# Performance work log

Hardware: AMD Instinct MI355X
Metric: run time of the kernel (lower is better)

Reference implementation:

```python
import jax, jax.numpy as jnp
import numpy as np

B, A, F, T = 4096, 64, 124, 8
H1, H2 = 64, 16


def setup_inputs() -> dict:
    key = jax.random.key(0)
    ks = jax.random.split(key, 10)
    x = jax.random.normal(ks[0], (B, A, F + 1), dtype=jnp.float32)
    types = jax.random.randint(ks[1], (B, A), 0, T).astype(jnp.float32)
    x = x.at[:, :, 0].set(types)  # column 0 stores atom-type index
    mask = (jax.random.uniform(ks[2], (B, A)) < 0.9).astype(jnp.float32)
    s1 = 1.0 / np.sqrt(F)
    s2 = 1.0 / np.sqrt(H1)
    s3 = 1.0 / np.sqrt(H2)
    return {
        "x_padded": x,
        "mask": mask,
        "W1": jax.random.normal(ks[3], (T, F, H1), dtype=jnp.float32) * s1,
        "b1": jax.random.normal(ks[4], (T, H1), dtype=jnp.float32) * s1,
        "W2": jax.random.normal(ks[5], (T, H1, H2), dtype=jnp.float32) * s2,
        "b2": jax.random.normal(ks[6], (T, H2), dtype=jnp.float32) * s2,
        "W3": jax.random.normal(ks[7], (T, H2, 1), dtype=jnp.float32) * s3,
        "b3": jax.random.normal(ks[8], (T, 1), dtype=jnp.float32) * s3,
    }


def reference(x_padded, mask, W1, b1, W2, b2, W3, b3):
    # x_padded: [B, A, 1+F]; mask: [B, A]
    type_idx = x_padded[:, :, 0].astype(jnp.int32)           # [B, A]
    feats = x_padded[:, :, 1:]                               # [B, A, F]
    n_types = W1.shape[0]
    # Faithful to the original: every type's subnet runs on the FULL batch
    # with non-matching atoms zero-masked (bias paths still contribute).
    type_mask = (type_idx[None, :, :] == jnp.arange(n_types)[:, None, None]).astype(feats.dtype)  # [T,B,A]
    sel = feats[None, :, :, :] * type_mask[..., None]        # [T,B,A,F]
    h = jax.nn.relu(jnp.einsum('tbaf,tfh->tbah', sel, W1) + b1[:, None, None, :])
    h = jax.nn.relu(jnp.einsum('tbah,thg->tbag', h, W2) + b2[:, None, None, :])
    o = jnp.einsum('tbag,tgo->tbao', h, W3) + b3[:, None, None, :]  # [T,B,A,1]
    per_atom = (o[..., 0] * mask[None, :, :]).sum(axis=0)   # [B, A]
    return per_atom.sum(axis=1, keepdims=True)               # [B, 1]
```

## Files before the change

### kernel.cpp

```cpp
#include <hip/hip_runtime.h>
#include <stdint.h>

#define NMOL 4096
#define NATOMS (NMOL * 64)
#define NF 124
#define NT 8
#define ROWV 125
#define CAP 65536

#define WS_DCONST  0
#define WS_CURSOR  64
#define WS_W1S     128
#define WS_W2T     131200
#define WS_LIST    147712

#define HS 72

typedef __attribute__((ext_vector_type(8))) short short8;
typedef __attribute__((ext_vector_type(4))) float floatx4;
typedef __attribute__((ext_vector_type(4), aligned(4))) float floatx4u;
typedef __attribute__((ext_vector_type(4))) unsigned int uint4v;

__device__ __forceinline__ unsigned short f2bf(float f) {
    unsigned u = __builtin_bit_cast(unsigned, f);
    u += 0x7fffu + ((u >> 16) & 1u);
    return (unsigned short)(u >> 16);
}
__device__ __forceinline__ unsigned pk2(float a, float b) {
    return (unsigned)f2bf(a) | ((unsigned)f2bf(b) << 16);
}
__device__ __forceinline__ void ld_lds16(const void* g, void* lds) {
    __builtin_amdgcn_global_load_lds(
        (const __attribute__((address_space(1))) unsigned int*)g,
        (__attribute__((address_space(3))) unsigned int*)lds, 16, 0, 0);
}

__global__ __launch_bounds__(256) void k_setup(const float* __restrict__ W1,
                                               const float* __restrict__ b1,
                                               const float* __restrict__ W2,
                                               const float* __restrict__ b2,
                                               const float* __restrict__ W3,
                                               const float* __restrict__ b3,
                                               float* __restrict__ dconst,
                                               unsigned* __restrict__ cursor,
                                               unsigned short* __restrict__ W1S,
                                               unsigned short* __restrict__ W2T,
                                               float* __restrict__ out) {
    int tid = threadIdx.x, b = blockIdx.x;
    if (b == 0) {
        __shared__ float c[NT];
        if (tid < 128) {
            int t = tid >> 4, g = tid & 15;
            float acc = b2[t * 16 + g];
            for (int h = 0; h < 64; ++h) {
                float h1 = b1[t * 64 + h];
                h1 = h1 > 0.f ? h1 : 0.f;
                acc += h1 * W2[(size_t)t * 1024 + h * 16 + g];
            }
            float h2 = acc > 0.f ? acc : 0.f;
            float v = h2 * W3[t * 16 + g];
            #pragma unroll
            for (int off = 1; off < 16; off <<= 1) v += __shfl_xor(v, off);
            if (g == 0) c[t] = v + b3[t];
        }
        if (tid < NT) cursor[tid] = (unsigned)(tid * CAP);
        __syncthreads();
        if (tid == 0) {
            float T_ = 0.f;
            for (int i = 0; i < NT; ++i) T_ += c[i];
            for (int i = 0; i < NT; ++i) dconst[i] = T_ - c[i] + b3[i];
        }
    } else if (b <= 8) {
        int t = b - 1;
        const float* w1g = W1 + (size_t)t * NF * 64;
        unsigned short* dst = W1S + (size_t)t * 8192;
        for (int id = tid; id < 1024; id += 256) {
            int h = id >> 4, cc = id & 15;
            unsigned u[4];
            #pragma unroll
            for (int j = 0; j < 4; ++j) {
                int f0 = cc * 8 + 2 * j;
                unsigned short lo = (f0 < NF)     ? f2bf(w1g[f0 * 64 + h])       : (unsigned short)0;
                unsigned short hi = (f0 + 1 < NF) ? f2bf(w1g[(f0 + 1) * 64 + h]) : (unsigned short)0;
                u[j] = (unsigned)lo | ((unsigned)hi << 16);
            }
            int p = cc ^ (h & 15);
            *(uint4v*)(dst + h * 128 + p * 8) = (uint4v){u[0], u[1], u[2], u[3]};
        }
        unsigned short* d2 = W2T + (size_t)t * 1024;
        for (int i = tid; i < 1024; i += 256) {
            int g = i >> 6, h = i & 63;
            d2[i] = f2bf(W2[(size_t)t * 1024 + h * 16 + g]);
        }
    } else {
        out[(b - 9) * 256 + tid] = 0.0f;
    }
}

__global__ __launch_bounds__(256) void k_sort(const float* __restrict__ x,
                                              const float* __restrict__ mask,
                                              unsigned* __restrict__ cursor,
                                              unsigned* __restrict__ list) {
    __shared__ unsigned scnt[2][4][NT];
    __shared__ unsigned sbase[2][4][NT];
    int tid = threadIdx.x;
    int wv = tid >> 6, lane = tid & 63;
    int base = blockIdx.x * 512;

    int ty_[2];
    unsigned long long mym[2];
    #pragma unroll
    for (int i = 0; i < 2; ++i) {
        int atom = base + i * 256 + tid;
        float tf = x[(size_t)atom * ROWV];
        float m  = mask[atom];
        int tt = (m != 0.0f) ? (int)tf : -1;
        ty_[i] = tt;
        unsigned long long bm = 0ull;
        unsigned mycnt = 0;
        #pragma unroll
        for (int ty = 0; ty < NT; ++ty) {
            unsigned long long b = __ballot(tt == ty);
            if (ty == tt) bm = b;
            if (lane == ty) mycnt = (unsigned)__popcll(b);
        }
        mym[i] = bm;
        if (lane < NT) scnt[i][wv][lane] = mycnt;
    }
    __syncthreads();
    if (tid < NT) {
        unsigned tot = 0;
        #pragma unroll
        for (int i = 0; i < 2; ++i)
            #pragma unroll
            for (int w = 0; w < 4; ++w) tot += scnt[i][w][tid];
        unsigned run = atomicAdd(&cursor[tid], tot);
        #pragma unroll
        for (int i = 0; i < 2; ++i)
            #pragma unroll
            for (int w = 0; w < 4; ++w) { sbase[i][w][tid] = run; run += scnt[i][w][tid]; }
    }
    __syncthreads();
    #pragma unroll
    for (int i = 0; i < 2; ++i) {
        int tt = ty_[i];
        if (tt >= 0) {
            unsigned rank = (unsigned)__popcll(mym[i] & ((1ull << lane) - 1ull));
            list[sbase[i][wv][tt] + rank] = (unsigned)(base + i * 256 + tid);
        }
    }
}

__global__ __launch_bounds__(256, 4) void k_mlp(const float* __restrict__ x,
                                                const unsigned short* __restrict__ W1S,
                                                const float* __restrict__ b1,
                                                const unsigned short* __restrict__ W2T,
                                                const float* __restrict__ b2,
                                                const float* __restrict__ W3,
                                                const unsigned* __restrict__ cursor,
                                                const float* __restrict__ dconst,
                                                const unsigned* __restrict__ list,
                                                float* __restrict__ out) {
    __shared__ unsigned short sW[64 * 128];
    __shared__ unsigned short sH[128 * HS];

    int t    = blockIdx.x >> 9;
    int tile = blockIdx.x & 511;
    int cnt  = (int)(cursor[t] - (unsigned)(t * CAP));
    int valid = cnt - (tile << 7);
    if (valid <= 0) return;
    if (valid > 128) valid = 128;
    int rowstart = t * CAP + (tile << 7);

    int tid  = threadIdx.x;
    int wv   = tid >> 6;
    int lane = tid & 63;
    int quad = lane >> 4, l15 = lane & 15;
    int rowbase = wv * 32;

    {
        const char* src = (const char*)W1S + (size_t)t * 16384 + wv * 4096 + lane * 16;
        char*       dst = (char*)sW + wv * 4096;
        #pragma unroll
        for (int i = 0; i < 4; ++i) ld_lds16(src + i * 1024, dst + i * 1024);
    }

    unsigned aid[2];
    #pragma unroll
    for (int m = 0; m < 2; ++m) {
        int row = rowbase + m * 16 + l15;
        aid[m] = list[rowstart + (row < valid ? row : 0)];
    }

    float b1v[4];
    #pragma unroll
    for (int n = 0; n < 4; ++n) b1v[n] = b1[t * 64 + n * 16 + l15];
    const unsigned short* w2t = W2T + (size_t)t * 1024;
    short8 bw2[2];
    #pragma unroll
    for (int ks = 0; ks < 2; ++ks)
        bw2[ks] = *(const short8*)(w2t + l15 * 64 + ks * 32 + quad * 8);
    float b2v = b2[t * 16 + l15];
    float w3v = W3[t * 16 + l15];
    float dct = dconst[t];

    short8 afrag[2][4];
    #pragma unroll
    for (int m = 0; m < 2; ++m) {
        const float* rp = x + (size_t)aid[m] * ROWV + 1;
        #pragma unroll
        for (int ks = 0; ks < 4; ++ks) {
            int k0 = ks * 32 + quad * 8;
            floatx4 f0 = (floatx4)(*(const floatx4u*)(rp + k0));
            floatx4 f1 = (floatx4)0.f;
            if (!(ks == 3 && quad == 3))
                f1 = (floatx4)(*(const floatx4u*)(rp + k0 + 4));
            uint4v uu = (uint4v){pk2(f0[0], f0[1]), pk2(f0[2], f0[3]),
                                 pk2(f1[0], f1[1]), pk2(f1[2], f1[3])};
            afrag[m][ks] = __builtin_bit_cast(short8, uu);
        }
    }

    __syncthreads();

    floatx4 c1[2][4];
    #pragma unroll
    for (int m = 0; m < 2; ++m)
        #pragma unroll
        for (int n = 0; n < 4; ++n) c1[m][n] = (floatx4)0.f;

    #pragma unroll
    for (int ks = 0; ks < 4; ++ks) {
        short8 bf[4];
        #pragma unroll
        for (int n = 0; n < 4; ++n)
            bf[n] = *(const short8*)(sW + (n * 16 + l15) * 128 + (((ks * 4 + quad) ^ l15) << 3));
        #pragma unroll
        for (int n = 0; n < 4; ++n) {
            c1[0][n] = __builtin_amdgcn_mfma_f32_16x16x32_bf16(afrag[0][ks], bf[n], c1[0][n], 0, 0, 0);
            c1[1][n] = __builtin_amdgcn_mfma_f32_16x16x32_bf16(afrag[1][ks], bf[n], c1[1][n], 0, 0, 0);
        }
    }

    #pragma unroll
    for (int m = 0; m < 2; ++m)
        #pragma unroll
        for (int n = 0; n < 4; ++n) {
            int col = n * 16 + l15;
            #pragma unroll
            for (int r = 0; r < 4; ++r) {
                float v = c1[m][n][r] + b1v[n];
                v = v > 0.f ? v : 0.f;
                sH[(rowbase + m * 16 + quad * 4 + r) * HS + col] = f2bf(v);
            }
        }

    floatx4 c2[2];
    c2[0] = (floatx4)0.f; c2[1] = (floatx4)0.f;
    #pragma unroll
    for (int ks = 0; ks < 2; ++ks) {
        int ko = ks * 32 + quad * 8;
        short8 a0 = *(const short8*)(sH + (rowbase + l15) * HS + ko);
        short8 a1 = *(const short8*)(sH + (rowbase + 16 + l15) * HS + ko);
        c2[0] = __builtin_amdgcn_mfma_f32_16x16x32_bf16(a0, bw2[ks], c2[0], 0, 0, 0);
        c2[1] = __builtin_amdgcn_mfma_f32_16x16x32_bf16(a1, bw2[ks], c2[1], 0, 0, 0);
    }

    #pragma unroll
    for (int m = 0; m < 2; ++m) {
        float h2v[4];
        #pragma unroll
        for (int r = 0; r < 4; ++r) {
            float v = c2[m][r] + b2v;
            v = v > 0.f ? v : 0.f;
            h2v[r] = v * w3v;
        }
        #pragma unroll
        for (int off = 1; off < 16; off <<= 1)
            #pragma unroll
            for (int r = 0; r < 4; ++r) h2v[r] += __shfl_xor(h2v[r], off);
        if (l15 == 0) {
            #pragma unroll
            for (int r = 0; r < 4; ++r) {
                int row = rowbase + m * 16 + quad * 4 + r;
                if (row < valid) {
                    unsigned atom = list[rowstart + row];
                    atomicAdd(&out[atom >> 6], h2v[r] + dct);
                }
            }
        }
    }
}

extern "C" void kernel_launch(void* const* d_in, const int* in_sizes, int n_in,
                              void* d_out, int out_size, void* d_ws, size_t ws_size,
                              hipStream_t stream) {
    const float* x    = (const float*)d_in[0];
    const float* mask = (const float*)d_in[1];
    const float* W1   = (const float*)d_in[2];
    const float* b1   = (const float*)d_in[3];
    const float* W2   = (const float*)d_in[4];
    const float* b2   = (const float*)d_in[5];
    const float* W3   = (const float*)d_in[6];
    const float* b3   = (const float*)d_in[7];
    float* out = (float*)d_out;

    char* ws = (char*)d_ws;
    float*          dconst = (float*)(ws + WS_DCONST);
    unsigned*       cursor = (unsigned*)(ws + WS_CURSOR);
    unsigned short* W1S    = (unsigned short*)(ws + WS_W1S);
    unsigned short* W2T    = (unsigned short*)(ws + WS_W2T);
    unsigned*       list   = (unsigned*)(ws + WS_LIST);

    k_setup<<<25, 256, 0, stream>>>(W1, b1, W2, b2, W3, b3, dconst, cursor, W1S, W2T, out);
    k_sort<<<512, 256, 0, stream>>>(x, mask, cursor, list);
    k_mlp<<<NT * (CAP / 128), 256, 0, stream>>>(x, W1S, b1, W2T, b2, W3,
                                                cursor, dconst, list, out);
}
```

Before: 224.0 us.

## Read W1 fragments directly from global, spread setup and sort over more blocks

```diff
diff --git a/kernel.cpp b/kernel.cpp
--- a/kernel.cpp
+++ b/kernel.cpp
@@ -28,11 +28,6 @@
 }
 __device__ __forceinline__ unsigned pk2(float a, float b) {
     return (unsigned)f2bf(a) | ((unsigned)f2bf(b) << 16);
-}
-__device__ __forceinline__ void ld_lds16(const void* g, void* lds) {
-    __builtin_amdgcn_global_load_lds(
-        (const __attribute__((address_space(1))) unsigned int*)g,
-        (__attribute__((address_space(3))) unsigned int*)lds, 16, 0, 0);
 }
 
 __global__ __launch_bounds__(256) void k_setup(const float* __restrict__ W1,
@@ -70,11 +65,12 @@
             for (int i = 0; i < NT; ++i) T_ += c[i];
             for (int i = 0; i < NT; ++i) dconst[i] = T_ - c[i] + b3[i];
         }
-    } else if (b <= 8) {
-        int t = b - 1;
+    } else if (b <= 32) {
+        int t = (b - 1) >> 2, sub = (b - 1) & 3;
         const float* w1g = W1 + (size_t)t * NF * 64;
         unsigned short* dst = W1S + (size_t)t * 8192;
-        for (int id = tid; id < 1024; id += 256) {
+        {
+            int id = sub * 256 + tid;
             int h = id >> 4, cc = id & 15;
             unsigned u[4];
             #pragma unroll
@@ -84,16 +80,15 @@
                 unsigned short hi = (f0 + 1 < NF) ? f2bf(w1g[(f0 + 1) * 64 + h]) : (unsigned short)0;
                 u[j] = (unsigned)lo | ((unsigned)hi << 16);
             }
-            int p = cc ^ (h & 15);
-            *(uint4v*)(dst + h * 128 + p * 8) = (uint4v){u[0], u[1], u[2], u[3]};
-        }
-        unsigned short* d2 = W2T + (size_t)t * 1024;
-        for (int i = tid; i < 1024; i += 256) {
+            *(uint4v*)(dst + h * 128 + cc * 8) = (uint4v){u[0], u[1], u[2], u[3]};
+        }
+        {
+            int i = sub * 256 + tid;
             int g = i >> 6, h = i & 63;
-            d2[i] = f2bf(W2[(size_t)t * 1024 + h * 16 + g]);
+            W2T[(size_t)t * 1024 + i] = f2bf(W2[(size_t)t * 1024 + h * 16 + g]);
         }
     } else {
-        out[(b - 9) * 256 + tid] = 0.0f;
+        out[(b - 33) * 256 + tid] = 0.0f;
     }
 }
 
@@ -101,53 +96,38 @@
                                               const float* __restrict__ mask,
                                               unsigned* __restrict__ cursor,
                                               unsigned* __restrict__ list) {
-    __shared__ unsigned scnt[2][4][NT];
-    __shared__ unsigned sbase[2][4][NT];
+    __shared__ unsigned scnt[4][NT];
+    __shared__ unsigned sbase[4][NT];
     int tid = threadIdx.x;
     int wv = tid >> 6, lane = tid & 63;
-    int base = blockIdx.x * 512;
-
-    int ty_[2];
-    unsigned long long mym[2];
-    #pragma unroll
-    for (int i = 0; i < 2; ++i) {
-        int atom = base + i * 256 + tid;
-        float tf = x[(size_t)atom * ROWV];
-        float m  = mask[atom];
-        int tt = (m != 0.0f) ? (int)tf : -1;
-        ty_[i] = tt;
-        unsigned long long bm = 0ull;
-        unsigned mycnt = 0;
-        #pragma unroll
-        for (int ty = 0; ty < NT; ++ty) {
-            unsigned long long b = __ballot(tt == ty);
-            if (ty == tt) bm = b;
-            if (lane == ty) mycnt = (unsigned)__popcll(b);
-        }
-        mym[i] = bm;
-        if (lane < NT) scnt[i][wv][lane] = mycnt;
-    }
+    int atom = blockIdx.x * 256 + tid;
+
+    float tf = x[(size_t)atom * ROWV];
+    float m  = mask[atom];
+    int tt = (m != 0.0f) ? (int)tf : -1;
+
+    unsigned long long bm = 0ull;
+    unsigned mycnt = 0;
+    #pragma unroll
+    for (int ty = 0; ty < NT; ++ty) {
+        unsigned long long b = __ballot(tt == ty);
+        if (ty == tt) bm = b;
+        if (lane == ty) mycnt = (unsigned)__popcll(b);
+    }
+    if (lane < NT) scnt[wv][lane] = mycnt;
     __syncthreads();
     if (tid < NT) {
         unsigned tot = 0;
         #pragma unroll
-        for (int i = 0; i < 2; ++i)
-            #pragma unroll
-            for (int w = 0; w < 4; ++w) tot += scnt[i][w][tid];
+        for (int w = 0; w < 4; ++w) tot += scnt[w][tid];
         unsigned run = atomicAdd(&cursor[tid], tot);
         #pragma unroll
-        for (int i = 0; i < 2; ++i)
-            #pragma unroll
-            for (int w = 0; w < 4; ++w) { sbase[i][w][tid] = run; run += scnt[i][w][tid]; }
+        for (int w = 0; w < 4; ++w) { sbase[w][tid] = run; run += scnt[w][tid]; }
     }
     __syncthreads();
-    #pragma unroll
-    for (int i = 0; i < 2; ++i) {
-        int tt = ty_[i];
-        if (tt >= 0) {
-            unsigned rank = (unsigned)__popcll(mym[i] & ((1ull << lane) - 1ull));
-            list[sbase[i][wv][tt] + rank] = (unsigned)(base + i * 256 + tid);
-        }
+    if (tt >= 0) {
+        unsigned rank = (unsigned)__popcll(bm & ((1ull << lane) - 1ull));
+        list[sbase[wv][tt] + rank] = (unsigned)atom;
     }
 }
 
@@ -161,7 +141,6 @@
                                                 const float* __restrict__ dconst,
                                                 const unsigned* __restrict__ list,
                                                 float* __restrict__ out) {
-    __shared__ unsigned short sW[64 * 128];
     __shared__ unsigned short sH[128 * HS];
 
     int t    = blockIdx.x >> 9;
@@ -177,13 +156,6 @@
     int lane = tid & 63;
     int quad = lane >> 4, l15 = lane & 15;
     int rowbase = wv * 32;
-
-    {
-        const char* src = (const char*)W1S + (size_t)t * 16384 + wv * 4096 + lane * 16;
-        char*       dst = (char*)sW + wv * 4096;
-        #pragma unroll
-        for (int i = 0; i < 4; ++i) ld_lds16(src + i * 1024, dst + i * 1024);
-    }
 
     unsigned aid[2];
     #pragma unroll
@@ -221,8 +193,7 @@
         }
     }
 
-    __syncthreads();
-
+    const unsigned short* w1t = W1S + (size_t)t * 8192;
     floatx4 c1[2][4];
     #pragma unroll
     for (int m = 0; m < 2; ++m)
@@ -234,7 +205,7 @@
         short8 bf[4];
         #pragma unroll
         for (int n = 0; n < 4; ++n)
-            bf[n] = *(const short8*)(sW + (n * 16 + l15) * 128 + (((ks * 4 + quad) ^ l15) << 3));
+            bf[n] = *(const short8*)(w1t + (n * 16 + l15) * 128 + (ks * 4 + quad) * 8);
         #pragma unroll
         for (int n = 0; n < 4; ++n) {
             c1[0][n] = __builtin_amdgcn_mfma_f32_16x16x32_bf16(afrag[0][ks], bf[n], c1[0][n], 0, 0, 0);
@@ -312,8 +283,8 @@
     unsigned short* W2T    = (unsigned short*)(ws + WS_W2T);
     unsigned*       list   = (unsigned*)(ws + WS_LIST);
 
-    k_setup<<<25, 256, 0, stream>>>(W1, b1, W2, b2, W3, b3, dconst, cursor, W1S, W2T, out);
-    k_sort<<<512, 256, 0, stream>>>(x, mask, cursor, list);
+    k_setup<<<49, 256, 0, stream>>>(W1, b1, W2, b2, W3, b3, dconst, cursor, W1S, W2T, out);
+    k_sort<<<1024, 256, 0, stream>>>(x, mask, cursor, list);
     k_mlp<<<NT * (CAP / 128), 256, 0, stream>>>(x, W1S, b1, W2T, b2, W3,
                                                 cursor, dconst, list, out);
 }
```

Measured after the change: 240.4 us. 7.3% more time.
